# Performance work log

Hardware: AMD Instinct MI355X
Metric: run time of the kernel (lower is better)

## Reference

```python
import jax, jax.numpy as jnp
import numpy as np

B, T, D = 2, 2048, 1024
H = 16
HD = D // H  # head dim == config.k == config.v == 64


def setup_inputs() -> dict:
    key = jax.random.key(0)
    k1, k2, k3 = jax.random.split(key, 3)
    scale = 0.02
    x = jax.random.normal(k1, (B, T, D), dtype=jnp.float32)
    W1 = jax.random.normal(k2, (D, 3 * D), dtype=jnp.float32) * scale
    b1 = jnp.zeros((3 * D,), dtype=jnp.float32)
    W2 = jax.random.normal(k3, (D, D), dtype=jnp.float32) * scale
    b2 = jnp.zeros((D,), dtype=jnp.float32)
    return {"x": x, "W1": W1, "b1": b1, "W2": W2, "b2": b2}


def reference(x, W1, b1, W2, b2):
    # Fused QKV projection (dropout layers are identity in eval mode).
    Bx, Tx, C = x.shape
    qkv = x @ W1 + b1                      # [B, T, 3D]
    q, k, v = jnp.split(qkv, 3, axis=-1)   # each [B, T, D]
    q = q.reshape(Bx, Tx, H, HD).transpose(0, 2, 1, 3)  # [B, H, T, hd]
    k = k.reshape(Bx, Tx, H, HD).transpose(0, 2, 1, 3)
    v = v.reshape(Bx, Tx, H, HD).transpose(0, 2, 1, 3)

    logits = jnp.einsum('bhmk,bhnk->bhmn', q, k) / jnp.sqrt(jnp.float32(HD))
    # causal mask (lower-triangular bias buffer)
    causal = jnp.tril(jnp.ones((Tx, Tx), dtype=bool))
    logits = jnp.where(causal[None, None], logits, jnp.float32(-jnp.inf))
    att = jax.nn.softmax(logits, axis=-1)   # [B, H, T, T]

    y = jnp.einsum('bhmn,bhnv->bhmv', att, v)        # [B, H, T, hd]
    y = y.transpose(0, 2, 1, 3).reshape(Bx, Tx, C)   # [B, T, D]
    return y @ W2 + b2
```

## Files before the change

### kernel.cpp

```cpp
#include <hip/hip_runtime.h>

typedef __attribute__((ext_vector_type(8))) short bf16x8;
typedef __attribute__((ext_vector_type(4))) float f32x4;
typedef __attribute__((ext_vector_type(16))) float f32x16;
typedef __attribute__((ext_vector_type(4))) short short4v;
typedef __attribute__((ext_vector_type(4))) unsigned int uint4v;

#define B_  2
#define T_  2048
#define D_  1024
#define H_  16
#define HD_ 64

__device__ inline short f2bf(float f){
  unsigned u = __builtin_bit_cast(unsigned, f);
  u += 0x7fff + ((u >> 16) & 1);
  return (short)(u >> 16);
}

__device__ inline void gl2lds16(const void* g, void* l){
  __builtin_amdgcn_global_load_lds(
      (const __attribute__((address_space(1))) unsigned int*)g,
      (__attribute__((address_space(3))) unsigned int*)l, 16, 0, 0);
}

__device__ inline void transpose_tile(const float* __restrict__ in,
                                      short* __restrict__ out,
                                      int R, int C, int bx, int by){
  __shared__ float tile[32][33];
  int tx = threadIdx.x & 31, ty0 = threadIdx.x >> 5;
#pragma unroll
  for (int i = 0; i < 4; i++){
    int ty = ty0 + i * 8;
    tile[ty][tx] = in[(by + ty) * C + bx + tx];
  }
  __syncthreads();
#pragma unroll
  for (int i = 0; i < 4; i++){
    int ty = ty0 + i * 8;
    out[(bx + ty) * R + by + tx] = f2bf(tile[tx][ty]);
  }
}

__global__ __launch_bounds__(256) void prep(
    const float* __restrict__ x,  short* __restrict__ xb,
    const float* __restrict__ W1, short* __restrict__ W1T,
    const float* __restrict__ W2, short* __restrict__ W2T){
  const int bid = blockIdx.x;
  if (bid < 4096){
    int i = (bid * 256 + threadIdx.x) * 4;
    float4 v = *(const float4*)(x + i);
    short4v o;
    o[0] = f2bf(v.x); o[1] = f2bf(v.y); o[2] = f2bf(v.z); o[3] = f2bf(v.w);
    *(short4v*)(xb + i) = o;
  } else if (bid < 4096 + 3072){
    int tb = bid - 4096;
    transpose_tile(W1, W1T, 1024, 3072, (tb % 96) << 5, (tb / 96) << 5);
  } else {
    int tb = bid - 7168;
    transpose_tile(W2, W2T, 1024, 1024, (tb % 32) << 5, (tb / 32) << 5);
  }
}

#define BM 128
#define BK 32

#define QSCALE 0.18033688011112042f

template<int N_, int K_, int EPI, int BN_, int TPB>
__global__ __launch_bounds__(TPB, 4) void gemm_bt(
    const short* __restrict__ A, const short* __restrict__ Bt,
    const float* __restrict__ bias,
    short* __restrict__ q, short* __restrict__ kk, short* __restrict__ vT,
    float* __restrict__ outf){
  constexpr int NWX = BN_ / 64;
  constexpr int LA  = (BM * 64) / (TPB * 16);
  constexpr int LB  = (BN_ * 64) / (TPB * 16);
  __shared__ short As[2][BM * BK];
  __shared__ short Bs[2][BN_ * BK];
  const int tid = threadIdx.x;
  const int lane = tid & 63, w = tid >> 6;
  const int wm = w / NWX, wn = w % NWX;
  const int lr = lane & 15, lk = lane >> 4;
  const int brow = blockIdx.y * BM, bcol = blockIdx.x * BN_;
  f32x4 acc[4][4] = {};
  const short* Ag = A  + brow * K_;
  const short* Bg = Bt + bcol * K_;

  auto stage = [&](int buf, int k0){
#pragma unroll
    for (int i = 0; i < LA; i++){
      int idx = i * TPB + tid;
      int row = idx >> 2, c8 = (idx & 3) * 8;
      gl2lds16(Ag + row * K_ + k0 + c8, (char*)As[buf] + idx * 16);
    }
#pragma unroll
    for (int i = 0; i < LB; i++){
      int idx = i * TPB + tid;
      int row = idx >> 2, c8 = (idx & 3) * 8;
      gl2lds16(Bg + row * K_ + k0 + c8, (char*)Bs[buf] + idx * 16);
    }
  };

  const int NT = K_ / BK;
  stage(0, 0);
  for (int t = 0; t < NT; ++t){
    const int cur = t & 1;
    if (t + 1 < NT){
      stage(cur ^ 1, (t + 1) * BK);
      if constexpr (LA + LB == 3)
        asm volatile("s_waitcnt vmcnt(3)" ::: "memory");
      else
        asm volatile("s_waitcnt vmcnt(4)" ::: "memory");
    } else {
      asm volatile("s_waitcnt vmcnt(0)" ::: "memory");
    }
    __builtin_amdgcn_s_barrier();
    __builtin_amdgcn_sched_barrier(0);

    bf16x8 a[4], b[4];
#pragma unroll
    for (int mf = 0; mf < 4; mf++)
      a[mf] = *(const bf16x8*)(As[cur] + (wm * 64 + mf * 16 + lr) * BK + lk * 8);
#pragma unroll
    for (int nf = 0; nf < 4; nf++)
      b[nf] = *(const bf16x8*)(Bs[cur] + (wn * 64 + nf * 16 + lr) * BK + lk * 8);
    __builtin_amdgcn_s_setprio(1);
#pragma unroll
    for (int mf = 0; mf < 4; mf++)
#pragma unroll
      for (int nf = 0; nf < 4; nf++)
        acc[mf][nf] = __builtin_amdgcn_mfma_f32_16x16x32_bf16(a[mf], b[nf], acc[mf][nf], 0, 0, 0);
    __builtin_amdgcn_s_setprio(0);
    __builtin_amdgcn_sched_barrier(0);
    __builtin_amdgcn_s_barrier();
  }

  if constexpr (EPI == 0){
#pragma unroll
    for (int nf = 0; nf < 4; nf++){
      int n = bcol + wn * 64 + nf * 16 + lr;
      float bv = bias[n];
      int sec = n >> 10, d = n & 1023, h = d >> 6, hd = d & 63;
#pragma unroll
      for (int mf = 0; mf < 4; mf++){
        int m0 = brow + wm * 64 + mf * 16 + lk * 4;
        int b = m0 >> 11, t0 = m0 & 2047;
        int bh = b * H_ + h;
        if (sec == 0){
#pragma unroll
          for (int r = 0; r < 4; r++)
            q[(bh * T_ + t0 + r) * HD_ + hd] = f2bf((acc[mf][nf][r] + bv) * QSCALE);
        } else if (sec == 1){
#pragma unroll
          for (int r = 0; r < 4; r++)
            kk[(bh * T_ + t0 + r) * HD_ + hd] = f2bf(acc[mf][nf][r] + bv);
        } else {
          float v0 = acc[mf][nf][0] + bv, v1 = acc[mf][nf][1] + bv;
          float v2 = acc[mf][nf][2] + bv, v3 = acc[mf][nf][3] + bv;
          unsigned lo = (unsigned)(unsigned short)f2bf(v0) | ((unsigned)(unsigned short)f2bf(v1) << 16);
          unsigned hi = (unsigned)(unsigned short)f2bf(v2) | ((unsigned)(unsigned short)f2bf(v3) << 16);
          uint2 pk; pk.x = lo; pk.y = hi;
          *(uint2*)(vT + (bh * HD_ + hd) * T_ + t0) = pk;
        }
      }
    }
  } else {
#pragma unroll
    for (int nf = 0; nf < 4; nf++){
      int n = bcol + wn * 64 + nf * 16 + lr;
      float bv = bias[n];
#pragma unroll
      for (int mf = 0; mf < 4; mf++){
        int m0 = brow + wm * 64 + mf * 16 + lk * 4;
#pragma unroll
        for (int r = 0; r < 4; r++)
          outf[(m0 + r) * N_ + n] = acc[mf][nf][r] + bv;
      }
    }
  }
}

__device__ inline int crow(int r, int h){ return (r & 3) + 8 * (r >> 2) + 4 * h; }

template<int SPLIT>
__global__ __launch_bounds__(256, 4) void attn32(
    const short* __restrict__ Q, const short* __restrict__ Kg,
    const short* __restrict__ Vt, short* __restrict__ Y,
    float* __restrict__ Op, float* __restrict__ ml){
  __shared__ short Ks[2][64 * 64];
  __shared__ short Vs[2][64 * 64];
  __shared__ float bounce[4][32];
  const int tid = threadIdx.x;
  const int w = tid >> 6, l = tid & 63;
  const int lq = l & 31, h = l >> 5;
  const int bx = blockIdx.x;
  int i, hf;
  if constexpr (SPLIT){
    int u = bx >> 5, v = u & 15;
    i = (v < 8) ? 15 - v : v - 8;
    hf = u >> 4;
  } else {
    i = (bx < 256) ? 15 - (bx >> 5) : (bx >> 5) - 8;
    hf = 0;
  }
  const int bh = bx & 31;
  const int q0 = i * 128, qw = q0 + w * 32;
  const int t0 = (SPLIT && hf) ? (i + 1) : 0;
  const int t1 = (SPLIT && !hf) ? (i + 1) : 2 * (i + 1);

  bf16x8 qb[4];
  {
    const short* qbase = Q + (bh * T_ + qw + lq) * HD_;
#pragma unroll
    for (int dk = 0; dk < 4; dk++)
      qb[dk] = *(const bf16x8*)(qbase + dk * 16 + h * 8);
  }

  f32x16 o0 = {}, o1 = {};
  float m = -1e30f, ll = 0.f;

  auto stage = [&](int buf, int t){
#pragma unroll
    for (int j = 0; j < 2; j++){
      int idx = j * 256 + tid;
      int row = idx >> 3, cb = (idx & 7) * 16;
      int cbs = cb ^ ((row & 7) << 4);
      gl2lds16(Kg + (bh * T_ + t * 64 + row) * HD_ + (cbs >> 1), (char*)Ks[buf] + idx * 16);
      gl2lds16(Vt + (bh * HD_ + row) * T_ + t * 64 + (cbs >> 1), (char*)Vs[buf] + idx * 16);
    }
  };

  stage(0, t0);
  for (int t = t0; t < t1; ++t){
    const int cur = (t - t0) & 1;
    if (t + 1 < t1){
      stage(cur ^ 1, t + 1);
      asm volatile("s_waitcnt vmcnt(4)" ::: "memory");
    } else {
      asm volatile("s_waitcnt vmcnt(0)" ::: "memory");
    }
    __builtin_amdgcn_s_barrier();
    __builtin_amdgcn_sched_barrier(0);

    const int kvb = t * 64;
    if (kvb <= qw + 31){
      const short* Kc = Ks[cur];
      const short* Vc = Vs[cur];

      f32x16 s[2] = {};
      __builtin_amdgcn_s_setprio(1);
#pragma unroll
      for (int kb = 0; kb < 2; kb++){
        int row = kb * 32 + lq;
        const char* rp = (const char*)Kc + row * 128;
        int swz = (row & 7) << 4;
#pragma unroll
        for (int dk = 0; dk < 4; dk++){
          bf16x8 ka = *(const bf16x8*)(rp + ((dk * 32 + h * 16) ^ swz));
          s[kb] = __builtin_amdgcn_mfma_f32_32x32x16_bf16(ka, qb[dk], s[kb], 0, 0, 0);
        }
      }
      __builtin_amdgcn_s_setprio(0);

      const int qg = qw + lq;
      if (kvb + 63 > qw){
#pragma unroll
        for (int kb = 0; kb < 2; kb++)
#pragma unroll
          for (int r = 0; r < 16; r++){
            int kv = kvb + kb * 32 + crow(r, h);
            if (kv > qg) s[kb][r] = -1e30f;
          }
      }

      float pm = s[0][0];
#pragma unroll
      for (int r = 1; r < 16; r++) pm = fmaxf(pm, s[0][r]);
#pragma unroll
      for (int r = 0; r < 16; r++) pm = fmaxf(pm, s[1][r]);
      pm = fmaxf(pm, __shfl_xor(pm, 32));

      if (__any(pm > m + 8.f)){
        float mn = fmaxf(pm, m);
        float sf = __builtin_amdgcn_exp2f(m - mn);
        m = mn;
        ll *= sf;
        bounce[w][lq] = sf;
#pragma unroll
        for (int r = 0; r < 16; r++){
          float sr = bounce[w][crow(r, h)];
          o0[r] *= sr; o1[r] *= sr;
        }
      }

      float ts = 0.f;
#pragma unroll
      for (int kb = 0; kb < 2; kb++)
#pragma unroll
        for (int r = 0; r < 16; r++){
          float p = __builtin_amdgcn_exp2f(s[kb][r] - m);
          s[kb][r] = p;
          ts += p;
        }
      ts += __shfl_xor(ts, 32);
      ll += ts;

      unsigned pw0[8], pw1[8];
#pragma unroll
      for (int kb = 0; kb < 2; kb++)
#pragma unroll
        for (int gg = 0; gg < 4; gg++){
          unsigned r0, r1;
          asm("v_cvt_pk_bf16_f32 %0, %1, %2" : "=v"(r0) : "v"(s[kb][gg * 4 + 0]), "v"(s[kb][gg * 4 + 1]));
          asm("v_cvt_pk_bf16_f32 %0, %1, %2" : "=v"(r1) : "v"(s[kb][gg * 4 + 2]), "v"(s[kb][gg * 4 + 3]));
          pw0[kb * 4 + gg] = r0;
          pw1[kb * 4 + gg] = r1;
        }
#pragma unroll
      for (int ks = 0; ks < 4; ks++){
        asm("v_permlane32_swap_b32 %0, %1" : "+v"(pw0[2 * ks]), "+v"(pw0[2 * ks + 1]));
        asm("v_permlane32_swap_b32 %0, %1" : "+v"(pw1[2 * ks]), "+v"(pw1[2 * ks + 1]));
      }

      __builtin_amdgcn_s_setprio(1);
#pragma unroll
      for (int ks = 0; ks < 4; ks++){
        uint4v paw;
        paw[0] = pw0[2 * ks];     paw[1] = pw1[2 * ks];
        paw[2] = pw0[2 * ks + 1]; paw[3] = pw1[2 * ks + 1];
        bf16x8 pa = __builtin_bit_cast(bf16x8, paw);
#pragma unroll
        for (int nb = 0; nb < 2; nb++){
          int row = nb * 32 + lq;
          bf16x8 vb = *(const bf16x8*)((const char*)Vc + row * 128 +
                        ((ks * 32 + h * 16) ^ ((row & 7) << 4)));
          if (nb == 0) o0 = __builtin_amdgcn_mfma_f32_32x32x16_bf16(pa, vb, o0, 0, 0, 0);
          else         o1 = __builtin_amdgcn_mfma_f32_32x32x16_bf16(pa, vb, o1, 0, 0, 0);
        }
      }
      __builtin_amdgcn_s_setprio(0);
    }
    __builtin_amdgcn_sched_barrier(0);
    __builtin_amdgcn_s_barrier();
  }

  if constexpr (SPLIT){
    float* Oq = Op + ((size_t)(hf * 32 + bh)) * (size_t)T_ * 64;
    if (h == 0){
      float* mlr = ml + ((size_t)(hf * 32 + bh) * T_ + (qw + lq)) * 2;
      mlr[0] = m; mlr[1] = ll;
    }
#pragma unroll
    for (int r = 0; r < 16; r++){
      int qg = qw + crow(r, h);
      Oq[qg * 64 + lq]      = o0[r];
      Oq[qg * 64 + 32 + lq] = o1[r];
    }
  } else {
    bounce[w][lq] = __builtin_amdgcn_rcpf(ll);
    const int b = bh >> 4, hh = bh & 15;
#pragma unroll
    for (int r = 0; r < 16; r++){
      int row = crow(r, h);
      float rl = bounce[w][row];
      int qg = qw + row;
      short* yb = Y + (b * T_ + qg) * D_ + hh * 64;
      yb[lq]      = f2bf(o0[r] * rl);
      yb[32 + lq] = f2bf(o1[r] * rl);
    }
  }
}

__global__ __launch_bounds__(256) void attn_merge(
    const float* __restrict__ Op, const float* __restrict__ ml,
    short* __restrict__ Y){
  int gid = blockIdx.x * 256 + threadIdx.x;
  int rid = gid >> 2, c16 = (gid & 3) * 16;
  float m1 = ml[rid * 2],           l1 = ml[rid * 2 + 1];
  float m2 = ml[131072 + rid * 2],  l2 = ml[131072 + rid * 2 + 1];
  float M  = fmaxf(m1, m2);
  float f1 = __builtin_amdgcn_exp2f(m1 - M);
  float f2 = __builtin_amdgcn_exp2f(m2 - M);
  float rl = 1.f / (f1 * l1 + f2 * l2);
  f1 *= rl; f2 *= rl;
  const float4* O1 = (const float4*)(Op + (size_t)rid * 64 + c16);
  const float4* O2 = (const float4*)(Op + 4194304ull + (size_t)rid * 64 + c16);
  int bh = rid >> 11, t = rid & 2047;
  short* yb = Y + (((bh >> 4) * T_ + t) * D_) + (bh & 15) * 64 + c16;
#pragma unroll
  for (int j = 0; j < 4; j++){
    float4 a = O1[j], b = O2[j];
    short4v o;
    o[0] = f2bf(f1 * a.x + f2 * b.x);
    o[1] = f2bf(f1 * a.y + f2 * b.y);
    o[2] = f2bf(f1 * a.z + f2 * b.z);
    o[3] = f2bf(f1 * a.w + f2 * b.w);
    *(short4v*)(yb + j * 4) = o;
  }
}

extern "C" void kernel_launch(void* const* d_in, const int* in_sizes, int n_in,
                              void* d_out, int out_size, void* d_ws, size_t ws_size,
                              hipStream_t stream) {
  const float* x  = (const float*)d_in[0];
  const float* W1 = (const float*)d_in[1];
  const float* b1 = (const float*)d_in[2];
  const float* W2 = (const float*)d_in[3];
  const float* b2 = (const float*)d_in[4];
  float* out = (float*)d_out;

  char* ws = (char*)d_ws;
  short* W1T = (short*)(ws);
  short* W2T = (short*)(ws + 6291456);
  short* xb  = (short*)(ws + 8388608);
  short* q   = (short*)(ws + 16777216);
  short* kk  = (short*)(ws + 25165824);
  short* vT  = (short*)(ws + 33554432);
  float* Op  = (float*)(ws + 41943040);
  float* mlb = (float*)(ws + 41943040 + 33554432);
  short* y   = xb;

  const size_t need = 41943040ull + 33554432ull + 1048576ull;
  const bool split = ws_size >= need;

  prep<<<dim3(8192), dim3(256), 0, stream>>>(x, xb, W1, W1T, W2, W2T);
  gemm_bt<3072, 1024, 0, 256, 512><<<dim3(12, 32), dim3(512), 0, stream>>>(xb, W1T, b1, q, kk, vT, nullptr);
  if (split){
    attn32<1><<<dim3(1024), dim3(256), 0, stream>>>(q, kk, vT, nullptr, Op, mlb);
    attn_merge<<<dim3(1024), dim3(256), 0, stream>>>(Op, mlb, y);
  } else {
    attn32<0><<<dim3(512), dim3(256), 0, stream>>>(q, kk, vT, y, nullptr, nullptr);
  }
  gemm_bt<1024, 1024, 1, 128, 256><<<dim3(8, 32), dim3(256), 0, stream>>>(y, W2T, b2, nullptr, nullptr, nullptr, out);
}
```

Measured before the change: 117.8 us.

## Use triple-buffered LDS pipeline with one barrier per K-step in GEMMs

Both GEMM kernels move from double to triple buffering in shared memory. The next-next tile is issued right after the barrier, and the trailing barrier at the end of each iteration is removed, so each K-step has one barrier. The QKV GEMM also changes from 128x256 tiles on 512 threads to 128x128 tiles on 256 threads, which doubles the grid to 768 blocks; launch bounds become 3 blocks per CU. This aims to hide global load latency and cut synchronisation, at the cost of 50% more LDS per block and less operand reuse per block in the QKV GEMM.

```diff
diff --git a/kernel.cpp b/kernel.cpp
--- a/kernel.cpp
+++ b/kernel.cpp
@@ -63,68 +63,61 @@
 }
 
 #define BM 128
+#define BN 128
 #define BK 32
 
 #define QSCALE 0.18033688011112042f
 
-template<int N_, int K_, int EPI, int BN_, int TPB>
-__global__ __launch_bounds__(TPB, 4) void gemm_bt(
+template<int N_, int K_, int EPI>
+__global__ __launch_bounds__(256, 3) void gemm_bt(
     const short* __restrict__ A, const short* __restrict__ Bt,
     const float* __restrict__ bias,
     short* __restrict__ q, short* __restrict__ kk, short* __restrict__ vT,
     float* __restrict__ outf){
-  constexpr int NWX = BN_ / 64;
-  constexpr int LA  = (BM * 64) / (TPB * 16);
-  constexpr int LB  = (BN_ * 64) / (TPB * 16);
-  __shared__ short As[2][BM * BK];
-  __shared__ short Bs[2][BN_ * BK];
+  __shared__ short As[3][BM * BK];
+  __shared__ short Bs[3][BN * BK];
   const int tid = threadIdx.x;
   const int lane = tid & 63, w = tid >> 6;
-  const int wm = w / NWX, wn = w % NWX;
+  const int wm = w >> 1, wn = w & 1;
   const int lr = lane & 15, lk = lane >> 4;
-  const int brow = blockIdx.y * BM, bcol = blockIdx.x * BN_;
+  const int brow = blockIdx.y * BM, bcol = blockIdx.x * BN;
   f32x4 acc[4][4] = {};
   const short* Ag = A  + brow * K_;
   const short* Bg = Bt + bcol * K_;
 
   auto stage = [&](int buf, int k0){
 #pragma unroll
-    for (int i = 0; i < LA; i++){
-      int idx = i * TPB + tid;
+    for (int i = 0; i < 2; i++){
+      int idx = i * 256 + tid;
       int row = idx >> 2, c8 = (idx & 3) * 8;
       gl2lds16(Ag + row * K_ + k0 + c8, (char*)As[buf] + idx * 16);
-    }
-#pragma unroll
-    for (int i = 0; i < LB; i++){
-      int idx = i * TPB + tid;
-      int row = idx >> 2, c8 = (idx & 3) * 8;
       gl2lds16(Bg + row * K_ + k0 + c8, (char*)Bs[buf] + idx * 16);
     }
   };
 
   const int NT = K_ / BK;
   stage(0, 0);
+  stage(1, BK);
   for (int t = 0; t < NT; ++t){
-    const int cur = t & 1;
-    if (t + 1 < NT){
-      stage(cur ^ 1, (t + 1) * BK);
-      if constexpr (LA + LB == 3)
-        asm volatile("s_waitcnt vmcnt(3)" ::: "memory");
-      else
-        asm volatile("s_waitcnt vmcnt(4)" ::: "memory");
-    } else {
+    if (t + 1 < NT)
+      asm volatile("s_waitcnt vmcnt(4)" ::: "memory");
+    else
       asm volatile("s_waitcnt vmcnt(0)" ::: "memory");
-    }
     __builtin_amdgcn_s_barrier();
     __builtin_amdgcn_sched_barrier(0);
-
+    if (t + 2 < NT)
+      stage((t + 2) % 3, (t + 2) * BK);
+    __builtin_amdgcn_sched_barrier(0);
+
+    const short* Ac = As[t % 3];
+    const short* Bc = Bs[t % 3];
     bf16x8 a[4], b[4];
 #pragma unroll
     for (int mf = 0; mf < 4; mf++)
-      a[mf] = *(const bf16x8*)(As[cur] + (wm * 64 + mf * 16 + lr) * BK + lk * 8);
+      a[mf] = *(const bf16x8*)(Ac + (wm * 64 + mf * 16 + lr) * BK + lk * 8);
 #pragma unroll
     for (int nf = 0; nf < 4; nf++)
-      b[nf] = *(const bf16x8*)(Bs[cur] + (wn * 64 + nf * 16 + lr) * BK + lk * 8);
+      b[nf] = *(const bf16x8*)(Bc + (wn * 64 + nf * 16 + lr) * BK + lk * 8);
     __builtin_amdgcn_s_setprio(1);
 #pragma unroll
     for (int mf = 0; mf < 4; mf++)
@@ -132,8 +125,6 @@
       for (int nf = 0; nf < 4; nf++)
         acc[mf][nf] = __builtin_amdgcn_mfma_f32_16x16x32_bf16(a[mf], b[nf], acc[mf][nf], 0, 0, 0);
     __builtin_amdgcn_s_setprio(0);
-    __builtin_amdgcn_sched_barrier(0);
-    __builtin_amdgcn_s_barrier();
   }
 
   if constexpr (EPI == 0){
@@ -425,12 +416,12 @@
   const bool split = ws_size >= need;
 
   prep<<<dim3(8192), dim3(256), 0, stream>>>(x, xb, W1, W1T, W2, W2T);
-  gemm_bt<3072, 1024, 0, 256, 512><<<dim3(12, 32), dim3(512), 0, stream>>>(xb, W1T, b1, q, kk, vT, nullptr);
+  gemm_bt<3072, 1024, 0><<<dim3(24, 32), dim3(256), 0, stream>>>(xb, W1T, b1, q, kk, vT, nullptr);
   if (split){
     attn32<1><<<dim3(1024), dim3(256), 0, stream>>>(q, kk, vT, nullptr, Op, mlb);
     attn_merge<<<dim3(1024), dim3(256), 0, stream>>>(Op, mlb, y);
   } else {
     attn32<0><<<dim3(512), dim3(256), 0, stream>>>(q, kk, vT, y, nullptr, nullptr);
   }
-  gemm_bt<1024, 1024, 1, 128, 256><<<dim3(8, 32), dim3(256), 0, stream>>>(y, W2T, b2, nullptr, nullptr, nullptr, out);
-}
+  gemm_bt<1024, 1024, 1><<<dim3(8, 32), dim3(256), 0, stream>>>(y, W2T, b2, nullptr, nullptr, nullptr, out);
+}
```

Result: no change. 116.2 us (-1.4%).
